# Kernel optimization log

Measured on AMD Instinct MI355X. Metric: run time of the kernel, lower is better.

## Reference

```python
import jax, jax.numpy as jnp
import numpy as np


def setup_inputs() -> dict:
    key = jax.random.key(0)
    kq, kk = jax.random.split(key)
    B, Q, K, D = 32, 512, 512, 1024
    queries = jax.random.normal(kq, (B, Q, D), dtype=jnp.float32)
    keys = jax.random.normal(kk, (B, K, D), dtype=jnp.float32)
    # ProbabilityConverter learned scalars (is_temperature=True, is_bias=True)
    temperature = jnp.ones((), dtype=jnp.float32)
    bias = jnp.zeros((), dtype=jnp.float32)
    return {"queries": queries, "keys": keys, "temperature": temperature, "bias": bias}


def reference(queries, keys, temperature, bias):
    # Dot scoring: (B, Q, D) x (B, K, D) -> (B, Q, K)
    logits = jnp.einsum("bqd,bkd->bqk", queries, keys)
    # keys.eq(0.0)[:, :, :1].transpose(1, 2): mask positions where first key feature == 0
    key_mask = (keys[:, :, 0] == 0.0)[:, None, :]  # (B, 1, K)
    neg_inf = jnp.array(-jnp.inf, dtype=logits.dtype)
    logits = jnp.where(key_mask, neg_inf, logits)
    # confidence = sigmoid((logsumexp(logits) + bias) * temperature)
    approx_max_logit = jax.nn.logsumexp(logits, axis=-1)  # (B, Q)
    confidence = jax.nn.sigmoid((approx_max_logit + bias) * temperature)
    attn = jax.nn.softmax(logits, axis=-1)  # (B, Q, K)
    return attn, confidence
```

## Files before the change

### kernel.cpp

```cpp
#include <hip/hip_runtime.h>
#include <math.h>


#define NB 32
#define NQ 512
#define NK 512
#define ND 1024
#define BM 64
#define BK 32
#define WCOLS 128

typedef __attribute__((ext_vector_type(8))) short short8;
typedef __attribute__((ext_vector_type(4))) float f32x4;

__device__ __forceinline__ void bf_split(float x, unsigned& hbits, float& lo) {
  unsigned u = __float_as_uint(x);
  unsigned r = u + 0x7fffu + ((u >> 16) & 1u);
  hbits = r & 0xffff0000u;
  lo = x - __uint_as_float(hbits);
}

__device__ __forceinline__ unsigned pack_rn(float x0, float x1) {
  unsigned u0 = __float_as_uint(x0), u1 = __float_as_uint(x1);
  unsigned r0 = u0 + 0x7fffu + ((u0 >> 16) & 1u);
  unsigned r1 = u1 + 0x7fffu + ((u1 >> 16) & 1u);
  return (r0 >> 16) | (r1 & 0xffff0000u);
}

__device__ __forceinline__ int lds_off_write(int r, int c4) {
  int slot = ((c4 >> 1) + (r >> 1)) & 3;
  return r * 32 + slot * 8 + (c4 & 1) * 4;
}
__device__ __forceinline__ int lds_off_read(int r, int quad) {
  int slot = (quad + (r >> 1)) & 3;
  return r * 32 + slot * 8;
}

__global__ __launch_bounds__(256, 1)
void attn_fused(const float* __restrict__ Qg, const float* __restrict__ Kg,
                const float* __restrict__ Tp, const float* __restrict__ Bp,
                float* __restrict__ attn, float* __restrict__ conf) {
  __shared__ __align__(16) unsigned short sAhi[BM * BK];
  __shared__ __align__(16) unsigned short sAlo[BM * BK];
  __shared__ __align__(16) unsigned short sBhi[NK * BK];
  __shared__ __align__(16) unsigned short sBlo[NK * BK];
  __shared__ float sRedA[4][BM];
  __shared__ float sRedB[4][BM];

  const int tid = threadIdx.x;
  const int g = blockIdx.x;
  const int batch = (g & 7) | (((g >> 3) & 3) << 3);
  const int q0 = (g >> 5) * BM;
  const int ln = tid & 63, w = tid >> 6;
  const int ln15 = ln & 15, quad = ln >> 4;
  const int wn0 = w * WCOLS;

  const float* Qp = Qg + ((size_t)batch * NQ + q0) * ND;
  const float* Kp = Kg + (size_t)batch * NK * ND;

  f32x4 acc[4][8];
#pragma unroll
  for (int mt = 0; mt < 4; ++mt)
#pragma unroll
    for (int nt = 0; nt < 8; ++nt)
      acc[mt][nt] = (f32x4){0.f, 0.f, 0.f, 0.f};

  float4 pb[16];
  float4 pa[2];
#pragma unroll
  for (int i = 0; i < 16; ++i) {
    int idx = tid + 256 * i;
    int r = idx >> 3, c4 = idx & 7;
    pb[i] = *(const float4*)(Kp + (size_t)r * ND + c4 * 4);
  }
#pragma unroll
  for (int i = 0; i < 2; ++i) {
    int idx = tid + 256 * i;
    int r = idx >> 3, c4 = idx & 7;
    pa[i] = *(const float4*)(Qp + (size_t)r * ND + c4 * 4);
  }

  for (int kt = 0; kt < ND / BK; ++kt) {
    if (kt) __syncthreads();

#pragma unroll
    for (int i = 0; i < 2; ++i) {
      int idx = tid + 256 * i;
      int r = idx >> 3, c4 = idx & 7;
      int off = lds_off_write(r, c4);
      float4 v = pa[i];
      unsigned h0, h1, h2, h3;
      float l0, l1, l2, l3;
      bf_split(v.x, h0, l0); bf_split(v.y, h1, l1);
      bf_split(v.z, h2, l2); bf_split(v.w, h3, l3);
      *(uint2*)(&sAhi[off]) = make_uint2((h0 >> 16) | h1, (h2 >> 16) | h3);
      *(uint2*)(&sAlo[off]) = make_uint2(pack_rn(l0, l1), pack_rn(l2, l3));
    }
#pragma unroll
    for (int i = 0; i < 16; ++i) {
      int idx = tid + 256 * i;
      int r = idx >> 3, c4 = idx & 7;
      int off = lds_off_write(r, c4);
      float4 v = pb[i];
      unsigned h0, h1, h2, h3;
      float l0, l1, l2, l3;
      bf_split(v.x, h0, l0); bf_split(v.y, h1, l1);
      bf_split(v.z, h2, l2); bf_split(v.w, h3, l3);
      *(uint2*)(&sBhi[off]) = make_uint2((h0 >> 16) | h1, (h2 >> 16) | h3);
      *(uint2*)(&sBlo[off]) = make_uint2(pack_rn(l0, l1), pack_rn(l2, l3));
    }
    __syncthreads();

    if (kt < ND / BK - 1) {
      const float* Kq = Kp + (kt + 1) * BK;
      const float* Qq = Qp + (kt + 1) * BK;
#pragma unroll
      for (int i = 0; i < 16; ++i) {
        int idx = tid + 256 * i;
        int r = idx >> 3, c4 = idx & 7;
        pb[i] = *(const float4*)(Kq + (size_t)r * ND + c4 * 4);
      }
#pragma unroll
      for (int i = 0; i < 2; ++i) {
        int idx = tid + 256 * i;
        int r = idx >> 3, c4 = idx & 7;
        pa[i] = *(const float4*)(Qq + (size_t)r * ND + c4 * 4);
      }
    }

    short8 ahi[4], alo[4];
#pragma unroll
    for (int mt = 0; mt < 4; ++mt) {
      int r = mt * 16 + ln15;
      int off = lds_off_read(r, quad);
      ahi[mt] = *(const short8*)(&sAhi[off]);
      alo[mt] = *(const short8*)(&sAlo[off]);
    }
#pragma unroll
    for (int nt = 0; nt < 8; ++nt) {
      int r = wn0 + nt * 16 + ln15;
      int off = lds_off_read(r, quad);
      short8 bhi = *(const short8*)(&sBhi[off]);
      short8 blo = *(const short8*)(&sBlo[off]);
#pragma unroll
      for (int mt = 0; mt < 4; ++mt) {
        acc[mt][nt] = __builtin_amdgcn_mfma_f32_16x16x32_bf16(ahi[mt], bhi, acc[mt][nt], 0, 0, 0);
        acc[mt][nt] = __builtin_amdgcn_mfma_f32_16x16x32_bf16(ahi[mt], blo, acc[mt][nt], 0, 0, 0);
        acc[mt][nt] = __builtin_amdgcn_mfma_f32_16x16x32_bf16(alo[mt], bhi, acc[mt][nt], 0, 0, 0);
      }
    }
  }

  const float NEGINF = -__builtin_inff();

  float rm[4][4];
#pragma unroll
  for (int mt = 0; mt < 4; ++mt)
#pragma unroll
    for (int rg = 0; rg < 4; ++rg) rm[mt][rg] = NEGINF;

#pragma unroll
  for (int nt = 0; nt < 8; ++nt) {
    int col = wn0 + nt * 16 + ln15;
    float kv = Kp[(size_t)col * ND];
    bool msk = (kv == 0.0f);
#pragma unroll
    for (int mt = 0; mt < 4; ++mt)
#pragma unroll
      for (int rg = 0; rg < 4; ++rg) {
        float v = msk ? NEGINF : acc[mt][nt][rg];
        acc[mt][nt][rg] = v;
        rm[mt][rg] = fmaxf(rm[mt][rg], v);
      }
  }
#pragma unroll
  for (int mt = 0; mt < 4; ++mt)
#pragma unroll
    for (int rg = 0; rg < 4; ++rg) {
      float v = rm[mt][rg];
#pragma unroll
      for (int d = 1; d < 16; d <<= 1) v = fmaxf(v, __shfl_xor(v, d, 64));
      rm[mt][rg] = v;
    }
  if (ln15 == 0) {
#pragma unroll
    for (int mt = 0; mt < 4; ++mt)
#pragma unroll
      for (int rg = 0; rg < 4; ++rg)
        sRedA[w][mt * 16 + quad * 4 + rg] = rm[mt][rg];
  }
  __syncthreads();

  float gmax[4][4], gsum[4][4];
#pragma unroll
  for (int mt = 0; mt < 4; ++mt)
#pragma unroll
    for (int rg = 0; rg < 4; ++rg) {
      int row = mt * 16 + quad * 4 + rg;
      gmax[mt][rg] = fmaxf(fmaxf(sRedA[0][row], sRedA[1][row]),
                           fmaxf(sRedA[2][row], sRedA[3][row]));
      gsum[mt][rg] = 0.f;
    }

#pragma unroll
  for (int nt = 0; nt < 8; ++nt)
#pragma unroll
    for (int mt = 0; mt < 4; ++mt)
#pragma unroll
      for (int rg = 0; rg < 4; ++rg) {
        float e = __expf(acc[mt][nt][rg] - gmax[mt][rg]);
        acc[mt][nt][rg] = e;
        gsum[mt][rg] += e;
      }
#pragma unroll
  for (int mt = 0; mt < 4; ++mt)
#pragma unroll
    for (int rg = 0; rg < 4; ++rg) {
      float v = gsum[mt][rg];
#pragma unroll
      for (int d = 1; d < 16; d <<= 1) v += __shfl_xor(v, d, 64);
      gsum[mt][rg] = v;
    }
  if (ln15 == 0) {
#pragma unroll
    for (int mt = 0; mt < 4; ++mt)
#pragma unroll
      for (int rg = 0; rg < 4; ++rg)
        sRedB[w][mt * 16 + quad * 4 + rg] = gsum[mt][rg];
  }
  __syncthreads();
#pragma unroll
  for (int mt = 0; mt < 4; ++mt)
#pragma unroll
    for (int rg = 0; rg < 4; ++rg) {
      int row = mt * 16 + quad * 4 + rg;
      gsum[mt][rg] = sRedB[0][row] + sRedB[1][row] + sRedB[2][row] + sRedB[3][row];
    }

  float* outBase = attn + ((size_t)batch * NQ + q0) * NK;
#pragma unroll
  for (int mt = 0; mt < 4; ++mt)
#pragma unroll
    for (int rg = 0; rg < 4; ++rg) {
      int row = mt * 16 + quad * 4 + rg;
      float inv = 1.0f / gsum[mt][rg];
#pragma unroll
      for (int nt = 0; nt < 8; ++nt) {
        int col = wn0 + nt * 16 + ln15;
        outBase[(size_t)row * NK + col] = acc[mt][nt][rg] * inv;
      }
    }

  if (w == 0 && ln15 == 0) {
    float tv = Tp[0], bv = Bp[0];
#pragma unroll
    for (int mt = 0; mt < 4; ++mt)
#pragma unroll
      for (int rg = 0; rg < 4; ++rg) {
        int row = mt * 16 + quad * 4 + rg;
        float lse = gmax[mt][rg] + __logf(gsum[mt][rg]);
        float t = (lse + bv) * tv;
        conf[(size_t)batch * NQ + q0 + row] = 1.0f / (1.0f + __expf(-t));
      }
  }
}

extern "C" void kernel_launch(void* const* d_in, const int* in_sizes, int n_in,
                              void* d_out, int out_size, void* d_ws, size_t ws_size,
                              hipStream_t stream) {
  const float* q = (const float*)d_in[0];
  const float* k = (const float*)d_in[1];
  const float* temp = (const float*)d_in[2];
  const float* bias = (const float*)d_in[3];
  float* attn = (float*)d_out;
  float* conf = attn + (size_t)NB * NQ * NK;

  dim3 grid(NB * (NQ / BM));
  dim3 block(256);
  hipLaunchKernelGGL(attn_fused, grid, block, 0, stream, q, k, temp, bias, attn, conf);
}
```

Measured before the change: 240.0 us.

## Pre-split K into bf16 hi/lo tiles in workspace and stream via global_load_lds

Adds a pre-pass kernel that converts each batch's K into swizzled bf16 hi/lo tiles, plus a mask vector, stored in the workspace. The main kernel then copies these tiles straight into LDS with global_load_lds, so K is no longer split again by every Q block. It also halves the Q tile to 32 rows so two blocks can share a CU. The cost is an extra launch and a workspace round trip, and the original kernel is kept as a fallback when the workspace is too small.

```diff
diff --git a/kernel.cpp b/kernel.cpp
--- a/kernel.cpp
+++ b/kernel.cpp
@@ -1,14 +1,19 @@
 #include <hip/hip_runtime.h>
 #include <math.h>
+#include <stdint.h>
 
 
 #define NB 32
 #define NQ 512
 #define NK 512
 #define ND 1024
-#define BM 64
 #define BK 32
-#define WCOLS 128
+#define NT (ND / BK)
+#define BM1 64
+#define BM2 32
+#define TILE_BYTES 65536
+#define WS_TILES ((size_t)NB * NT * TILE_BYTES)
+#define WS_TOTAL (WS_TILES + (size_t)NB * NK * 4)
 
 typedef __attribute__((ext_vector_type(8))) short short8;
 typedef __attribute__((ext_vector_type(4))) float f32x4;
@@ -19,7 +24,6 @@
   hbits = r & 0xffff0000u;
   lo = x - __uint_as_float(hbits);
 }
-
 __device__ __forceinline__ unsigned pack_rn(float x0, float x1) {
   unsigned u0 = __float_as_uint(x0), u1 = __float_as_uint(x1);
   unsigned r0 = u0 + 0x7fffu + ((u0 >> 16) & 1u);
@@ -36,24 +40,243 @@
   return r * 32 + slot * 8;
 }
 
-__global__ __launch_bounds__(256, 1)
-void attn_fused(const float* __restrict__ Qg, const float* __restrict__ Kg,
-                const float* __restrict__ Tp, const float* __restrict__ Bp,
-                float* __restrict__ attn, float* __restrict__ conf) {
-  __shared__ __align__(16) unsigned short sAhi[BM * BK];
-  __shared__ __align__(16) unsigned short sAlo[BM * BK];
+__device__ __forceinline__ void gl2lds16(const void* g, void* l) {
+  __builtin_amdgcn_global_load_lds(
+      (const __attribute__((address_space(1))) unsigned int*)g,
+      (__attribute__((address_space(3))) unsigned int*)l, 16, 0, 0);
+}
+
+__global__ __launch_bounds__(256)
+void convert_k(const float* __restrict__ Kg, unsigned char* __restrict__ ws) {
+  const int bx = blockIdx.x;
+  const int batch = bx >> 5, kt = bx & 31;
+  const float* src = Kg + (size_t)batch * NK * ND + kt * BK;
+  unsigned short* hiB = (unsigned short*)(ws + (size_t)bx * TILE_BYTES);
+  unsigned short* loB = hiB + 32768 / 2;
+  float* maskB = (float*)(ws + WS_TILES) + batch * NK;
+
+#pragma unroll
+  for (int i = 0; i < 16; ++i) {
+    int idx = threadIdx.x + 256 * i;
+    int r = idx >> 3, c4 = idx & 7;
+    float4 v = *(const float4*)(src + (size_t)r * ND + c4 * 4);
+    unsigned h0, h1, h2, h3;
+    float l0, l1, l2, l3;
+    bf_split(v.x, h0, l0); bf_split(v.y, h1, l1);
+    bf_split(v.z, h2, l2); bf_split(v.w, h3, l3);
+    int off = lds_off_write(r, c4);
+    *(uint2*)(&hiB[off]) = make_uint2((h0 >> 16) | h1, (h2 >> 16) | h3);
+    *(uint2*)(&loB[off]) = make_uint2(pack_rn(l0, l1), pack_rn(l2, l3));
+    if (kt == 0 && c4 == 0) maskB[r] = v.x;
+  }
+}
+
+__global__ __launch_bounds__(256, 2)
+void attn_fused_v2(const float* __restrict__ Qg,
+                   const unsigned char* __restrict__ ws,
+                   const float* __restrict__ Tp, const float* __restrict__ Bp,
+                   float* __restrict__ attn, float* __restrict__ conf) {
   __shared__ __align__(16) unsigned short sBhi[NK * BK];
   __shared__ __align__(16) unsigned short sBlo[NK * BK];
-  __shared__ float sRedA[4][BM];
-  __shared__ float sRedB[4][BM];
+  __shared__ __align__(16) unsigned short sAhi[BM2 * BK];
+  __shared__ __align__(16) unsigned short sAlo[BM2 * BK];
+  __shared__ float sRedA[4][BM2];
+  __shared__ float sRedB[4][BM2];
 
   const int tid = threadIdx.x;
   const int g = blockIdx.x;
   const int batch = (g & 7) | (((g >> 3) & 3) << 3);
-  const int q0 = (g >> 5) * BM;
+  const int q0 = (g >> 5) * BM2;
   const int ln = tid & 63, w = tid >> 6;
   const int ln15 = ln & 15, quad = ln >> 4;
-  const int wn0 = w * WCOLS;
+  const int wn0 = w * 128;
+
+  const float* Qp = Qg + ((size_t)batch * NQ + q0) * ND;
+  const unsigned char* wsB = ws + (size_t)batch * NT * TILE_BYTES;
+  const float* maskB = (const float*)(ws + WS_TILES) + batch * NK;
+
+  f32x4 acc[2][8];
+#pragma unroll
+  for (int mt = 0; mt < 2; ++mt)
+#pragma unroll
+    for (int nt = 0; nt < 8; ++nt) acc[mt][nt] = (f32x4){0.f, 0.f, 0.f, 0.f};
+
+  const int ar = tid >> 3, ac4 = tid & 7;
+  float4 pa = *(const float4*)(Qp + (size_t)ar * ND + ac4 * 4);
+
+  for (int kt = 0; kt < NT; ++kt) {
+    if (kt) __syncthreads();
+
+    const unsigned char* tb = wsB + (size_t)kt * TILE_BYTES;
+#pragma unroll
+    for (int c = 0; c < 8; ++c) {
+      int byte = (((c * 4 + w) * 64) + ln) * 16;
+      gl2lds16(tb + byte, ((unsigned char*)sBhi) + byte);
+      gl2lds16(tb + 32768 + byte, ((unsigned char*)sBlo) + byte);
+    }
+    {
+      unsigned h0, h1, h2, h3;
+      float l0, l1, l2, l3;
+      bf_split(pa.x, h0, l0); bf_split(pa.y, h1, l1);
+      bf_split(pa.z, h2, l2); bf_split(pa.w, h3, l3);
+      int off = lds_off_write(ar, ac4);
+      *(uint2*)(&sAhi[off]) = make_uint2((h0 >> 16) | h1, (h2 >> 16) | h3);
+      *(uint2*)(&sAlo[off]) = make_uint2(pack_rn(l0, l1), pack_rn(l2, l3));
+    }
+    __syncthreads();
+
+    if (kt + 1 < NT)
+      pa = *(const float4*)(Qp + (kt + 1) * BK + (size_t)ar * ND + ac4 * 4);
+
+    short8 ahi[2], alo[2];
+#pragma unroll
+    for (int mt = 0; mt < 2; ++mt) {
+      int off = lds_off_read(mt * 16 + ln15, quad);
+      ahi[mt] = *(const short8*)(&sAhi[off]);
+      alo[mt] = *(const short8*)(&sAlo[off]);
+    }
+#pragma unroll
+    for (int nt = 0; nt < 8; ++nt) {
+      int off = lds_off_read(wn0 + nt * 16 + ln15, quad);
+      short8 bhi = *(const short8*)(&sBhi[off]);
+      short8 blo = *(const short8*)(&sBlo[off]);
+#pragma unroll
+      for (int mt = 0; mt < 2; ++mt) {
+        acc[mt][nt] = __builtin_amdgcn_mfma_f32_16x16x32_bf16(ahi[mt], bhi, acc[mt][nt], 0, 0, 0);
+        acc[mt][nt] = __builtin_amdgcn_mfma_f32_16x16x32_bf16(ahi[mt], blo, acc[mt][nt], 0, 0, 0);
+        acc[mt][nt] = __builtin_amdgcn_mfma_f32_16x16x32_bf16(alo[mt], bhi, acc[mt][nt], 0, 0, 0);
+      }
+    }
+  }
+
+  const float NEGINF = -__builtin_inff();
+  float rm[2][4];
+#pragma unroll
+  for (int mt = 0; mt < 2; ++mt)
+#pragma unroll
+    for (int rg = 0; rg < 4; ++rg) rm[mt][rg] = NEGINF;
+
+#pragma unroll
+  for (int nt = 0; nt < 8; ++nt) {
+    int col = wn0 + nt * 16 + ln15;
+    bool msk = (maskB[col] == 0.0f);
+#pragma unroll
+    for (int mt = 0; mt < 2; ++mt)
+#pragma unroll
+      for (int rg = 0; rg < 4; ++rg) {
+        float v = msk ? NEGINF : acc[mt][nt][rg];
+        acc[mt][nt][rg] = v;
+        rm[mt][rg] = fmaxf(rm[mt][rg], v);
+      }
+  }
+#pragma unroll
+  for (int mt = 0; mt < 2; ++mt)
+#pragma unroll
+    for (int rg = 0; rg < 4; ++rg) {
+      float v = rm[mt][rg];
+#pragma unroll
+      for (int d = 1; d < 16; d <<= 1) v = fmaxf(v, __shfl_xor(v, d, 64));
+      rm[mt][rg] = v;
+    }
+  if (ln15 == 0) {
+#pragma unroll
+    for (int mt = 0; mt < 2; ++mt)
+#pragma unroll
+      for (int rg = 0; rg < 4; ++rg)
+        sRedA[w][mt * 16 + quad * 4 + rg] = rm[mt][rg];
+  }
+  __syncthreads();
+
+  float gmax[2][4], gsum[2][4];
+#pragma unroll
+  for (int mt = 0; mt < 2; ++mt)
+#pragma unroll
+    for (int rg = 0; rg < 4; ++rg) {
+      int row = mt * 16 + quad * 4 + rg;
+      gmax[mt][rg] = fmaxf(fmaxf(sRedA[0][row], sRedA[1][row]),
+                           fmaxf(sRedA[2][row], sRedA[3][row]));
+      gsum[mt][rg] = 0.f;
+    }
+
+#pragma unroll
+  for (int nt = 0; nt < 8; ++nt)
+#pragma unroll
+    for (int mt = 0; mt < 2; ++mt)
+#pragma unroll
+      for (int rg = 0; rg < 4; ++rg) {
+        float e = __expf(acc[mt][nt][rg] - gmax[mt][rg]);
+        acc[mt][nt][rg] = e;
+        gsum[mt][rg] += e;
+      }
+#pragma unroll
+  for (int mt = 0; mt < 2; ++mt)
+#pragma unroll
+    for (int rg = 0; rg < 4; ++rg) {
+      float v = gsum[mt][rg];
+#pragma unroll
+      for (int d = 1; d < 16; d <<= 1) v += __shfl_xor(v, d, 64);
+      gsum[mt][rg] = v;
+    }
+  if (ln15 == 0) {
+#pragma unroll
+    for (int mt = 0; mt < 2; ++mt)
+#pragma unroll
+      for (int rg = 0; rg < 4; ++rg)
+        sRedB[w][mt * 16 + quad * 4 + rg] = gsum[mt][rg];
+  }
+  __syncthreads();
+#pragma unroll
+  for (int mt = 0; mt < 2; ++mt)
+#pragma unroll
+    for (int rg = 0; rg < 4; ++rg) {
+      int row = mt * 16 + quad * 4 + rg;
+      gsum[mt][rg] = sRedB[0][row] + sRedB[1][row] + sRedB[2][row] + sRedB[3][row];
+    }
+
+  float* outBase = attn + ((size_t)batch * NQ + q0) * NK;
+#pragma unroll
+  for (int mt = 0; mt < 2; ++mt)
+#pragma unroll
+    for (int rg = 0; rg < 4; ++rg) {
+      int row = mt * 16 + quad * 4 + rg;
+      float inv = 1.0f / gsum[mt][rg];
+#pragma unroll
+      for (int nt = 0; nt < 8; ++nt)
+        outBase[(size_t)row * NK + wn0 + nt * 16 + ln15] = acc[mt][nt][rg] * inv;
+    }
+
+  if (w == 0 && ln15 == 0) {
+    float tv = Tp[0], bv = Bp[0];
+#pragma unroll
+    for (int mt = 0; mt < 2; ++mt)
+#pragma unroll
+      for (int rg = 0; rg < 4; ++rg) {
+        int row = mt * 16 + quad * 4 + rg;
+        float lse = gmax[mt][rg] + __logf(gsum[mt][rg]);
+        float t = (lse + bv) * tv;
+        conf[(size_t)batch * NQ + q0 + row] = 1.0f / (1.0f + __expf(-t));
+      }
+  }
+}
+
+__global__ __launch_bounds__(256, 1)
+void attn_fused_v1(const float* __restrict__ Qg, const float* __restrict__ Kg,
+                   const float* __restrict__ Tp, const float* __restrict__ Bp,
+                   float* __restrict__ attn, float* __restrict__ conf) {
+  __shared__ __align__(16) unsigned short sAhi[BM1 * BK];
+  __shared__ __align__(16) unsigned short sAlo[BM1 * BK];
+  __shared__ __align__(16) unsigned short sBhi[NK * BK];
+  __shared__ __align__(16) unsigned short sBlo[NK * BK];
+  __shared__ float sRedA[4][BM1];
+  __shared__ float sRedB[4][BM1];
+
+  const int tid = threadIdx.x;
+  const int g = blockIdx.x;
+  const int batch = (g & 7) | (((g >> 3) & 3) << 3);
+  const int q0 = (g >> 5) * BM1;
+  const int ln = tid & 63, w = tid >> 6;
+  const int ln15 = ln & 15, quad = ln >> 4;
+  const int wn0 = w * 128;
 
   const float* Qp = Qg + ((size_t)batch * NQ + q0) * ND;
   const float* Kp = Kg + (size_t)batch * NK * ND;
@@ -62,68 +285,55 @@
 #pragma unroll
   for (int mt = 0; mt < 4; ++mt)
 #pragma unroll
-    for (int nt = 0; nt < 8; ++nt)
-      acc[mt][nt] = (f32x4){0.f, 0.f, 0.f, 0.f};
-
-  float4 pb[16];
-  float4 pa[2];
+    for (int nt = 0; nt < 8; ++nt) acc[mt][nt] = (f32x4){0.f, 0.f, 0.f, 0.f};
+
+  float4 pb[16], pa[2];
 #pragma unroll
   for (int i = 0; i < 16; ++i) {
-    int idx = tid + 256 * i;
-    int r = idx >> 3, c4 = idx & 7;
+    int idx = tid + 256 * i, r = idx >> 3, c4 = idx & 7;
     pb[i] = *(const float4*)(Kp + (size_t)r * ND + c4 * 4);
   }
 #pragma unroll
   for (int i = 0; i < 2; ++i) {
-    int idx = tid + 256 * i;
-    int r = idx >> 3, c4 = idx & 7;
+    int idx = tid + 256 * i, r = idx >> 3, c4 = idx & 7;
     pa[i] = *(const float4*)(Qp + (size_t)r * ND + c4 * 4);
   }
 
-  for (int kt = 0; kt < ND / BK; ++kt) {
+  for (int kt = 0; kt < NT; ++kt) {
     if (kt) __syncthreads();
-
 #pragma unroll
     for (int i = 0; i < 2; ++i) {
-      int idx = tid + 256 * i;
-      int r = idx >> 3, c4 = idx & 7;
+      int idx = tid + 256 * i, r = idx >> 3, c4 = idx & 7;
       int off = lds_off_write(r, c4);
-      float4 v = pa[i];
-      unsigned h0, h1, h2, h3;
-      float l0, l1, l2, l3;
-      bf_split(v.x, h0, l0); bf_split(v.y, h1, l1);
-      bf_split(v.z, h2, l2); bf_split(v.w, h3, l3);
+      unsigned h0, h1, h2, h3; float l0, l1, l2, l3;
+      bf_split(pa[i].x, h0, l0); bf_split(pa[i].y, h1, l1);
+      bf_split(pa[i].z, h2, l2); bf_split(pa[i].w, h3, l3);
       *(uint2*)(&sAhi[off]) = make_uint2((h0 >> 16) | h1, (h2 >> 16) | h3);
       *(uint2*)(&sAlo[off]) = make_uint2(pack_rn(l0, l1), pack_rn(l2, l3));
     }
 #pragma unroll
     for (int i = 0; i < 16; ++i) {
-      int idx = tid + 256 * i;
-      int r = idx >> 3, c4 = idx & 7;
+      int idx = tid + 256 * i, r = idx >> 3, c4 = idx & 7;
       int off = lds_off_write(r, c4);
-      float4 v = pb[i];
-      unsigned h0, h1, h2, h3;
-      float l0, l1, l2, l3;
-      bf_split(v.x, h0, l0); bf_split(v.y, h1, l1);
-      bf_split(v.z, h2, l2); bf_split(v.w, h3, l3);
+      unsigned h0, h1, h2, h3; float l0, l1, l2, l3;
+      bf_split(pb[i].x, h0, l0); bf_split(pb[i].y, h1, l1);
+      bf_split(pb[i].z, h2, l2); bf_split(pb[i].w, h3, l3);
       *(uint2*)(&sBhi[off]) = make_uint2((h0 >> 16) | h1, (h2 >> 16) | h3);
       *(uint2*)(&sBlo[off]) = make_uint2(pack_rn(l0, l1), pack_rn(l2, l3));
     }
     __syncthreads();
 
-    if (kt < ND / BK - 1) {
+    if (kt < NT - 1) {
       const float* Kq = Kp + (kt + 1) * BK;
       const float* Qq = Qp + (kt + 1) * BK;
 #pragma unroll
       for (int i = 0; i < 16; ++i) {
-        int idx = tid + 256 * i;
-        int r = idx >> 3, c4 = idx & 7;
+        int idx = tid + 256 * i, r = idx >> 3, c4 = idx & 7;
         pb[i] = *(const float4*)(Kq + (size_t)r * ND + c4 * 4);
       }
 #pragma unroll
       for (int i = 0; i < 2; ++i) {
-        int idx = tid + 256 * i;
-        int r = idx >> 3, c4 = idx & 7;
+        int idx = tid + 256 * i, r = idx >> 3, c4 = idx & 7;
         pa[i] = *(const float4*)(Qq + (size_t)r * ND + c4 * 4);
       }
     }
@@ -131,15 +341,13 @@
     short8 ahi[4], alo[4];
 #pragma unroll
     for (int mt = 0; mt < 4; ++mt) {
-      int r = mt * 16 + ln15;
-      int off = lds_off_read(r, quad);
+      int off = lds_off_read(mt * 16 + ln15, quad);
       ahi[mt] = *(const short8*)(&sAhi[off]);
       alo[mt] = *(const short8*)(&sAlo[off]);
     }
 #pragma unroll
     for (int nt = 0; nt < 8; ++nt) {
-      int r = wn0 + nt * 16 + ln15;
-      int off = lds_off_read(r, quad);
+      int off = lds_off_read(wn0 + nt * 16 + ln15, quad);
       short8 bhi = *(const short8*)(&sBhi[off]);
       short8 blo = *(const short8*)(&sBlo[off]);
 #pragma unroll
@@ -152,18 +360,15 @@
   }
 
   const float NEGINF = -__builtin_inff();
-
   float rm[4][4];
 #pragma unroll
   for (int mt = 0; mt < 4; ++mt)
 #pragma unroll
     for (int rg = 0; rg < 4; ++rg) rm[mt][rg] = NEGINF;
-
 #pragma unroll
   for (int nt = 0; nt < 8; ++nt) {
     int col = wn0 + nt * 16 + ln15;
-    float kv = Kp[(size_t)col * ND];
-    bool msk = (kv == 0.0f);
+    bool msk = (Kp[(size_t)col * ND] == 0.0f);
 #pragma unroll
     for (int mt = 0; mt < 4; ++mt)
 #pragma unroll
@@ -182,13 +387,12 @@
       for (int d = 1; d < 16; d <<= 1) v = fmaxf(v, __shfl_xor(v, d, 64));
       rm[mt][rg] = v;
     }
-  if (ln15 == 0) {
+  if (ln15 == 0)
 #pragma unroll
     for (int mt = 0; mt < 4; ++mt)
 #pragma unroll
       for (int rg = 0; rg < 4; ++rg)
         sRedA[w][mt * 16 + quad * 4 + rg] = rm[mt][rg];
-  }
   __syncthreads();
 
   float gmax[4][4], gsum[4][4];
@@ -201,7 +405,6 @@
                            fmaxf(sRedA[2][row], sRedA[3][row]));
       gsum[mt][rg] = 0.f;
     }
-
 #pragma unroll
   for (int nt = 0; nt < 8; ++nt)
 #pragma unroll
@@ -221,13 +424,12 @@
       for (int d = 1; d < 16; d <<= 1) v += __shfl_xor(v, d, 64);
       gsum[mt][rg] = v;
     }
-  if (ln15 == 0) {
+  if (ln15 == 0)
 #pragma unroll
     for (int mt = 0; mt < 4; ++mt)
 #pragma unroll
       for (int rg = 0; rg < 4; ++rg)
         sRedB[w][mt * 16 + quad * 4 + rg] = gsum[mt][rg];
-  }
   __syncthreads();
 #pragma unroll
   for (int mt = 0; mt < 4; ++mt)
@@ -245,12 +447,9 @@
       int row = mt * 16 + quad * 4 + rg;
       float inv = 1.0f / gsum[mt][rg];
 #pragma unroll
-      for (int nt = 0; nt < 8; ++nt) {
-        int col = wn0 + nt * 16 + ln15;
-        outBase[(size_t)row * NK + col] = acc[mt][nt][rg] * inv;
-      }
-    }
-
+      for (int nt = 0; nt < 8; ++nt)
+        outBase[(size_t)row * NK + wn0 + nt * 16 + ln15] = acc[mt][nt][rg] * inv;
+    }
   if (w == 0 && ln15 == 0) {
     float tv = Tp[0], bv = Bp[0];
 #pragma unroll
@@ -275,7 +474,13 @@
   float* attn = (float*)d_out;
   float* conf = attn + (size_t)NB * NQ * NK;
 
-  dim3 grid(NB * (NQ / BM));
-  dim3 block(256);
-  hipLaunchKernelGGL(attn_fused, grid, block, 0, stream, q, k, temp, bias, attn, conf);
-}
+  if (ws_size >= WS_TOTAL) {
+    hipLaunchKernelGGL(convert_k, dim3(NB * NT), dim3(256), 0, stream,
+                       k, (unsigned char*)d_ws);
+    hipLaunchKernelGGL(attn_fused_v2, dim3(NB * (NQ / BM2)), dim3(256), 0, stream,
+                       q, (const unsigned char*)d_ws, temp, bias, attn, conf);
+  } else {
+    hipLaunchKernelGGL(attn_fused_v1, dim3(NB * (NQ / BM1)), dim3(256), 0, stream,
+                       q, k, temp, bias, attn, conf);
+  }
+}
```

Measured after the change: 226.9 us. -5.5%, faster.
